# Kernel optimization log

Measured on AMD Instinct MI355X. Metric: run time of the kernel, lower is better.

Reference implementation:

```python
import jax, jax.numpy as jnp
import numpy as np

N = 200_000      # nodes
DEG = 10         # edges per node (RadiusGraph max_num_neighbors=10, loop=True)
E = N * DEG
F0, F1 = 3, 20   # in features (pos), hidden
EPS = 1e-5       # PyG StdAggregation epsilon


def _glorot(k, shape):
    return jax.random.normal(k, shape, jnp.float32) / jnp.sqrt(jnp.float32(shape[-1]))


def setup_inputs() -> dict:
    key = jax.random.key(0)
    ks = jax.random.split(key, 20)
    x = jax.random.normal(ks[0], (N, F0), jnp.float32)
    # each node gets DEG incoming edges: dst structured, src random; first edge per node is a self-loop
    src = jax.random.randint(ks[1], (E,), 0, N, jnp.int32)
    dst = jnp.repeat(jnp.arange(N, dtype=jnp.int32), DEG)
    src = src.at[::DEG].set(jnp.arange(N, dtype=jnp.int32))  # self-loops
    edge_index = jnp.stack([src, dst])
    return {
        "x": x,
        "edge_index": edge_index,
        # conv1: PNAConv(3, 20)
        "w_pre1": _glorot(ks[2], (F0, 2 * F0)), "b_pre1": jnp.zeros((F0,), jnp.float32),
        "w_post1": _glorot(ks[3], (F1, 17 * F0)), "b_post1": jnp.zeros((F1,), jnp.float32),
        "w_lin1": _glorot(ks[4], (F1, F1)), "b_lin1": jnp.zeros((F1,), jnp.float32),
        # conv2: PNAConv(20, 20)
        "w_pre2": _glorot(ks[5], (F1, 2 * F1)), "b_pre2": jnp.zeros((F1,), jnp.float32),
        "w_post2": _glorot(ks[6], (F1, 17 * F1)), "b_post2": jnp.zeros((F1,), jnp.float32),
        "w_lin2": _glorot(ks[7], (F1, F1)), "b_lin2": jnp.zeros((F1,), jnp.float32),
        # final Linear(20, 1)
        "w_out": _glorot(ks[8], (1, F1)), "b_out": jnp.zeros((1,), jnp.float32),
    }


def _pna(x, src, dst, avg_lin, avg_log, w_pre, b_pre, w_post, b_post, w_lin, b_lin):
    n = x.shape[0]
    # message: pre_nn(x_i || x_j)
    h = jnp.concatenate([x[dst], x[src]], axis=-1)          # [E, 2F]
    m = h @ w_pre.T + b_pre                                 # [E, F]
    cnt = jax.ops.segment_sum(jnp.ones(dst.shape[0], jnp.float32), dst, num_segments=n)
    deg = jnp.maximum(cnt, 1.0)                             # [N]
    s = jax.ops.segment_sum(m, dst, num_segments=n)
    s2 = jax.ops.segment_sum(m * m, dst, num_segments=n)
    mean = s / deg[:, None]
    var = jax.nn.relu(s2 / deg[:, None] - mean * mean)
    std = jnp.sqrt(var + EPS)
    has = (cnt > 0.0)[:, None]
    mn = jnp.where(has, jax.ops.segment_min(m, dst, num_segments=n), 0.0)
    mx = jnp.where(has, jax.ops.segment_max(m, dst, num_segments=n), 0.0)
    agg = jnp.concatenate([mean, mn, mx, std], axis=-1)     # [N, 4F]
    # degree scalers: identity, amplification, attenuation, linear
    logd = jnp.log(deg + 1.0)[:, None]
    out = jnp.concatenate([agg,
                           agg * (logd / avg_log),
                           agg * (avg_log / logd),
                           agg * (deg / avg_lin)[:, None]], axis=-1)  # [N, 16F]
    out = jnp.concatenate([x, out], axis=-1)                # [N, 17F]
    out = out @ w_post.T + b_post                           # post_nn
    return out @ w_lin.T + b_lin                            # final tower mixer


def reference(x, edge_index, w_pre1, b_pre1, w_post1, b_post1, w_lin1, b_lin1,
              w_pre2, b_pre2, w_post2, b_post2, w_lin2, b_lin2, w_out, b_out):
    src, dst = edge_index[0], edge_index[1]
    n = x.shape[0]
    cnt = jax.ops.segment_sum(jnp.ones(dst.shape[0], jnp.float32), dst, num_segments=n)
    avg_lin = cnt.mean()                    # avg_deg['lin'] over the degree histogram
    avg_log = jnp.log(cnt + 1.0).mean()     # avg_deg['log']
    h = jax.nn.relu(_pna(x, src, dst, avg_lin, avg_log, w_pre1, b_pre1, w_post1, b_post1, w_lin1, b_lin1))
    h = jax.nn.relu(_pna(h, src, dst, avg_lin, avg_log, w_pre2, b_pre2, w_post2, b_post2, w_lin2, b_lin2))
    return h @ w_out.T + b_out              # [N, 1]
```

## Files before the change

### kernel.cpp

```cpp
#include <hip/hip_runtime.h>
#include <hip/hip_fp16.h>


#define N_NODES 200000
#define NPB 64
#define NBLK (N_NODES / NPB)

#define O_WD1  0
#define O_WA1  64
#define O_B1C  304
#define O_WD2  336
#define O_WA2  736
#define O_B2C  2336
#define O_B2H  4096
#define O_D2H  2004096

__global__ __launch_bounds__(128) void fold_kernel(
    const float* __restrict__ w_pre1, const float* __restrict__ b_pre1,
    const float* __restrict__ w_post1, const float* __restrict__ b_post1,
    const float* __restrict__ w_lin1,  const float* __restrict__ b_lin1,
    const float* __restrict__ w_pre2, const float* __restrict__ b_pre2,
    const float* __restrict__ w_post2, const float* __restrict__ b_post2,
    const float* __restrict__ w_lin2,  const float* __restrict__ b_lin2,
    float* __restrict__ ws)
{
    __shared__ float wl1[20], wl2[20], c1[51], c2s[340];
    __shared__ float swa1[12], swa2[80], s1[3], s2[20];
    const int j = blockIdx.x;
    const int t = threadIdx.x;
    if (t < 20) { wl1[t] = w_lin1[j*20 + t]; wl2[t] = w_lin2[j*20 + t]; }
    __syncthreads();
    for (int c = t; c < 51; c += 128) {
        float a = 0.f;
        #pragma unroll
        for (int k = 0; k < 20; ++k) a += wl1[k] * w_post1[k*51 + c];
        c1[c] = a;
    }
    for (int c = t; c < 340; c += 128) {
        float a = 0.f;
        #pragma unroll
        for (int k = 0; k < 20; ++k) a += wl2[k] * w_post2[k*340 + c];
        c2s[c] = a;
    }
    __syncthreads();
    if (t < 12) swa1[t] = c1[3+t]  + c1[15+t]  + c1[27+t]  + c1[39+t];
    if (t < 80) swa2[t] = c2s[20+t] + c2s[100+t] + c2s[180+t] + c2s[260+t];
    __syncthreads();
    if (t < 3)  s1[t] = swa1[t] + swa1[3+t]  + swa1[6+t];
    if (t < 20) s2[t] = swa2[t] + swa2[20+t] + swa2[40+t];
    if (t < 12) ws[O_WA1 + j*12 + t] = swa1[t];
    if (t < 80) ws[O_WA2 + j*80 + t] = swa2[t];
    __syncthreads();
    if (t < 3) {
        float a = c1[t];
        #pragma unroll
        for (int r = 0; r < 3; ++r) a += s1[r] * w_pre1[r*6 + t];
        ws[O_WD1 + j*3 + t] = a;
    }
    if (t < 20) {
        float a = c2s[t];
        #pragma unroll
        for (int r = 0; r < 20; ++r) a += s2[r] * w_pre2[r*40 + t];
        ws[O_WD2 + j*20 + t] = a;
    }
    if (t == 0) {
        float a = b_lin1[j];
        #pragma unroll
        for (int k = 0; k < 20; ++k) a += wl1[k] * b_post1[k];
        #pragma unroll
        for (int r = 0; r < 3;  ++r) a += s1[r] * b_pre1[r];
        ws[O_B1C + j] = a;
        float b = b_lin2[j];
        #pragma unroll
        for (int k = 0; k < 20; ++k) b += wl2[k] * b_post2[k];
        #pragma unroll
        for (int r = 0; r < 20; ++r) b += s2[r] * b_pre2[r];
        ws[O_B2C + j] = b;
    }
}

__global__ __launch_bounds__(320) void k1_kernel(
    const float* __restrict__ x, const int* __restrict__ src,
    const float* __restrict__ w_pre1, const float* __restrict__ w_pre2,
    const float* __restrict__ ws,
    __half* __restrict__ b2h, __half* __restrict__ d2h)
{
    __shared__ float sM[NPB * 33];
    __shared__ float sAgg[NPB * 13];
    __shared__ float sH1[NPB * 21];
    const int t = threadIdx.x;
    const int node0 = blockIdx.x * NPB;

    const int pil = t & 63;
    const float xi0 = x[(node0+pil)*3+0];
    const float xi1 = x[(node0+pil)*3+1];
    const float xi2 = x[(node0+pil)*3+2];

    #pragma unroll
    for (int p = 0; p < 2; ++p) {
        const int slot = p*320 + t;
        const int il = slot / 10, e = slot - il*10;
        const int sj = __builtin_nontemporal_load(&src[node0*10 + slot]);
        const float xs0 = x[sj*3+0], xs1 = x[sj*3+1], xs2 = x[sj*3+2];
        #pragma unroll
        for (int ff = 0; ff < 3; ++ff) {
            sM[il*33 + e*3 + ff] =
                w_pre1[ff*6+3]*xs0 + w_pre1[ff*6+4]*xs1 + w_pre1[ff*6+5]*xs2;
        }
    }
    __syncthreads();

    if (t < 192) {
        const int il = t / 3, f = t - il*3;
        float sum = 0.f, sq = 0.f, mn = 1e30f, mx = -1e30f;
        #pragma unroll
        for (int e = 0; e < 10; ++e) {
            const float m = sM[il*33 + e*3 + f];
            sum += m; sq += m*m; mn = fminf(mn, m); mx = fmaxf(mx, m);
        }
        const float mean = sum * 0.1f;
        const float var  = fmaxf(sq * 0.1f - mean*mean, 0.f);
        sAgg[il*13 + 0 + f] = mean;
        sAgg[il*13 + 3 + f] = mn;
        sAgg[il*13 + 6 + f] = mx;
        sAgg[il*13 + 9 + f] = sqrtf(var + 1e-5f);
    }
    __syncthreads();

    const int wv = __builtin_amdgcn_readfirstlane(t >> 6);
    const int il = t & 63;
    const int node = node0 + il;
    const int f0 = wv * 4;

    float ag[12];
    #pragma unroll
    for (int k = 0; k < 12; ++k) ag[k] = sAgg[il*13 + k];
    #pragma unroll
    for (int ff = 0; ff < 4; ++ff) {
        const int f = f0 + ff;
        float acc = ws[O_B1C + f]
            + ws[O_WD1 + f*3+0]*xi0 + ws[O_WD1 + f*3+1]*xi1 + ws[O_WD1 + f*3+2]*xi2;
        #pragma unroll
        for (int k = 0; k < 12; ++k) acc += ws[O_WA1 + f*12 + k] * ag[k];
        sH1[il*21 + f] = fmaxf(acc, 0.f);
    }
    __syncthreads();

    float hk[20];
    #pragma unroll
    for (int k = 0; k < 20; ++k) hk[k] = sH1[il*21 + k];
    float vb[4], vd[4];
    #pragma unroll
    for (int ff = 0; ff < 4; ++ff) {
        const int f = f0 + ff;
        float B = 0.f, D = ws[O_B2C + f];
        #pragma unroll
        for (int k = 0; k < 20; ++k) {
            B += w_pre2[f*40 + 20 + k] * hk[k];
            D += ws[O_WD2 + f*20 + k]  * hk[k];
        }
        vb[ff] = B; vd[ff] = D;
    }
    union { __half2 h[2]; unsigned long long u; } pb, pd;
    pb.h[0] = __floats2half2_rn(vb[0], vb[1]);
    pb.h[1] = __floats2half2_rn(vb[2], vb[3]);
    pd.h[0] = __floats2half2_rn(vd[0], vd[1]);
    pd.h[1] = __floats2half2_rn(vd[2], vd[3]);
    __builtin_nontemporal_store(pb.u, (unsigned long long*)&b2h[node*20 + f0]);
    __builtin_nontemporal_store(pd.u, (unsigned long long*)&d2h[node*20 + f0]);
}

__global__ __launch_bounds__(320) void k2_kernel(
    const int* __restrict__ src, const float* __restrict__ ws,
    const __half* __restrict__ b2h, const __half* __restrict__ d2h,
    const float* __restrict__ w_out, const float* __restrict__ b_out,
    float* __restrict__ out)
{
    __shared__ float sAgg[NPB * 81];
    __shared__ int   sSrc[NPB * 10];
    __shared__ float sPart[320];
    const int t = threadIdx.x;
    const int node0 = blockIdx.x * NPB;

    const int pil = t & 63;
    const int pf0 = (t >> 6) * 4;
    union { unsigned long long u; __half2 h[2]; } pdd;
    pdd.u = __builtin_nontemporal_load(
        (const unsigned long long*)&d2h[(node0+pil)*20 + pf0]);

    sSrc[t]       = __builtin_nontemporal_load(&src[node0*10 + t]);
    sSrc[320 + t] = __builtin_nontemporal_load(&src[node0*10 + 320 + t]);
    __syncthreads();

    #pragma unroll
    for (int p = 0; p < 2; ++p) {
        const int idx = p*320 + t;
        const int il = idx / 10, fp = idx - il*10;
        const int f = 2*fp;
        float s0=0.f, s1=0.f, q0=0.f, q1=0.f;
        float mn0=1e30f, mn1=1e30f, mx0=-1e30f, mx1=-1e30f;
        #pragma unroll
        for (int e = 0; e < 10; ++e) {
            const int sj = sSrc[il*10 + e];
            const float2 b = __half22float2(*(const __half2*)&b2h[sj*20 + f]);
            s0 += b.x; q0 += b.x*b.x; mn0 = fminf(mn0, b.x); mx0 = fmaxf(mx0, b.x);
            s1 += b.y; q1 += b.y*b.y; mn1 = fminf(mn1, b.y); mx1 = fmaxf(mx1, b.y);
        }
        const float me0 = s0*0.1f, me1 = s1*0.1f;
        const float sd0 = sqrtf(fmaxf(q0*0.1f - me0*me0, 0.f) + 1e-5f);
        const float sd1 = sqrtf(fmaxf(q1*0.1f - me1*me1, 0.f) + 1e-5f);
        sAgg[il*81 + f]      = me0;  sAgg[il*81 + f + 1]      = me1;
        sAgg[il*81 + 20 + f] = mn0;  sAgg[il*81 + 20 + f + 1] = mn1;
        sAgg[il*81 + 40 + f] = mx0;  sAgg[il*81 + 40 + f + 1] = mx1;
        sAgg[il*81 + 60 + f] = sd0;  sAgg[il*81 + 60 + f + 1] = sd1;
    }
    __syncthreads();

    const int wv = __builtin_amdgcn_readfirstlane(t >> 6);
    const int il = t & 63;
    const int f0 = wv * 4;

    const float2 d01 = __half22float2(pdd.h[0]);
    const float2 d23 = __half22float2(pdd.h[1]);
    float acc0 = d01.x, acc1 = d01.y, acc2 = d23.x, acc3 = d23.y;
    #pragma unroll
    for (int k = 0; k < 80; ++k) {
        const float ag = sAgg[il*81 + k];
        acc0 += ws[O_WA2 + (f0+0)*80 + k] * ag;
        acc1 += ws[O_WA2 + (f0+1)*80 + k] * ag;
        acc2 += ws[O_WA2 + (f0+2)*80 + k] * ag;
        acc3 += ws[O_WA2 + (f0+3)*80 + k] * ag;
    }
    const float py = w_out[f0+0]*fmaxf(acc0, 0.f) + w_out[f0+1]*fmaxf(acc1, 0.f)
                   + w_out[f0+2]*fmaxf(acc2, 0.f) + w_out[f0+3]*fmaxf(acc3, 0.f);
    sPart[wv*64 + il] = py;
    __syncthreads();

    if (t < 64) {
        float y = b_out[0];
        #pragma unroll
        for (int v = 0; v < 5; ++v) y += sPart[v*64 + t];
        __builtin_nontemporal_store(y, &out[node0 + t]);
    }
}

extern "C" void kernel_launch(void* const* d_in, const int* in_sizes, int n_in,
                              void* d_out, int out_size, void* d_ws, size_t ws_size,
                              hipStream_t stream)
{
    const float* x       = (const float*)d_in[0];
    const int*   eidx    = (const int*)  d_in[1];
    const float* w_pre1  = (const float*)d_in[2];
    const float* b_pre1  = (const float*)d_in[3];
    const float* w_post1 = (const float*)d_in[4];
    const float* b_post1 = (const float*)d_in[5];
    const float* w_lin1  = (const float*)d_in[6];
    const float* b_lin1  = (const float*)d_in[7];
    const float* w_pre2  = (const float*)d_in[8];
    const float* b_pre2  = (const float*)d_in[9];
    const float* w_post2 = (const float*)d_in[10];
    const float* b_post2 = (const float*)d_in[11];
    const float* w_lin2  = (const float*)d_in[12];
    const float* b_lin2  = (const float*)d_in[13];
    const float* w_out   = (const float*)d_in[14];
    const float* b_out   = (const float*)d_in[15];
    float* out = (float*)d_out;
    float* ws  = (float*)d_ws;
    __half* b2h = (__half*)(ws + O_B2H);
    __half* d2h = (__half*)(ws + O_D2H);

    fold_kernel<<<20, 128, 0, stream>>>(w_pre1, b_pre1, w_post1, b_post1,
                                        w_lin1, b_lin1, w_pre2, b_pre2,
                                        w_post2, b_post2, w_lin2, b_lin2, ws);
    k1_kernel<<<NBLK, 320, 0, stream>>>(x, eidx, w_pre1, w_pre2, ws, b2h, d2h);
    k2_kernel<<<NBLK, 320, 0, stream>>>(eidx, ws, b2h, d2h, w_out, b_out, out);
}
```

Baseline: 66.40 us.

## Double nodes per block and pad gathered half table rows to 64 bytes

Each block now handles 128 nodes instead of 64, with bounds checks for a partial tail block, so every thread processes two nodes and the weight loads are amortised over more work. The layer-2 gather table b2h is padded from 20 to 32 halves per node, so each neighbour row starts on a 64-byte boundary and the gather in k2 touches fewer cache lines. Nontemporal loads and stores are swapped for plain accesses. In exchange the gather table takes more memory and more store bandwidth, and the larger shared-memory footprint and fewer blocks may lower occupancy.

```diff
diff --git a/kernel.cpp b/kernel.cpp
--- a/kernel.cpp
+++ b/kernel.cpp
@@ -3,8 +3,8 @@
 
 
 #define N_NODES 200000
-#define NPB 64
-#define NBLK (N_NODES / NPB)
+#define NPB 128
+#define NBLK ((N_NODES + NPB - 1) / NPB)
 
 #define O_WD1  0
 #define O_WA1  64
@@ -13,7 +13,7 @@
 #define O_WA2  736
 #define O_B2C  2336
 #define O_B2H  4096
-#define O_D2H  2004096
+#define O_D2H  3204096
 
 __global__ __launch_bounds__(128) void fold_kernel(
     const float* __restrict__ w_pre1, const float* __restrict__ b_pre1,
@@ -90,84 +90,108 @@
     __shared__ float sH1[NPB * 21];
     const int t = threadIdx.x;
     const int node0 = blockIdx.x * NPB;
-
-    const int pil = t & 63;
-    const float xi0 = x[(node0+pil)*3+0];
-    const float xi1 = x[(node0+pil)*3+1];
-    const float xi2 = x[(node0+pil)*3+2];
+    const int nv = (N_NODES - node0 < NPB) ? (N_NODES - node0) : NPB;
+
+    float xi[2][3];
+    #pragma unroll
+    for (int h = 0; h < 2; ++h) {
+        const int n = node0 + h*64 + (t & 63);
+        if (n < N_NODES) {
+            xi[h][0] = x[n*3+0]; xi[h][1] = x[n*3+1]; xi[h][2] = x[n*3+2];
+        }
+    }
+
+    #pragma unroll
+    for (int p = 0; p < 4; ++p) {
+        const int slot = p*320 + t;
+        if (slot < nv*10) {
+            const int il = slot / 10, e = slot - il*10;
+            const int sj = src[node0*10 + slot];
+            const float xs0 = x[sj*3+0], xs1 = x[sj*3+1], xs2 = x[sj*3+2];
+            #pragma unroll
+            for (int ff = 0; ff < 3; ++ff) {
+                sM[il*33 + e*3 + ff] =
+                    w_pre1[ff*6+3]*xs0 + w_pre1[ff*6+4]*xs1 + w_pre1[ff*6+5]*xs2;
+            }
+        }
+    }
+    __syncthreads();
 
     #pragma unroll
     for (int p = 0; p < 2; ++p) {
-        const int slot = p*320 + t;
-        const int il = slot / 10, e = slot - il*10;
-        const int sj = __builtin_nontemporal_load(&src[node0*10 + slot]);
-        const float xs0 = x[sj*3+0], xs1 = x[sj*3+1], xs2 = x[sj*3+2];
-        #pragma unroll
-        for (int ff = 0; ff < 3; ++ff) {
-            sM[il*33 + e*3 + ff] =
-                w_pre1[ff*6+3]*xs0 + w_pre1[ff*6+4]*xs1 + w_pre1[ff*6+5]*xs2;
-        }
-    }
-    __syncthreads();
-
-    if (t < 192) {
-        const int il = t / 3, f = t - il*3;
-        float sum = 0.f, sq = 0.f, mn = 1e30f, mx = -1e30f;
-        #pragma unroll
-        for (int e = 0; e < 10; ++e) {
-            const float m = sM[il*33 + e*3 + f];
-            sum += m; sq += m*m; mn = fminf(mn, m); mx = fmaxf(mx, m);
-        }
-        const float mean = sum * 0.1f;
-        const float var  = fmaxf(sq * 0.1f - mean*mean, 0.f);
-        sAgg[il*13 + 0 + f] = mean;
-        sAgg[il*13 + 3 + f] = mn;
-        sAgg[il*13 + 6 + f] = mx;
-        sAgg[il*13 + 9 + f] = sqrtf(var + 1e-5f);
+        const int idx = p*320 + t;
+        if (idx < nv*3) {
+            const int il = idx / 3, f = idx - il*3;
+            float sum = 0.f, sq = 0.f, mn = 1e30f, mx = -1e30f;
+            #pragma unroll
+            for (int e = 0; e < 10; ++e) {
+                const float m = sM[il*33 + e*3 + f];
+                sum += m; sq += m*m; mn = fminf(mn, m); mx = fmaxf(mx, m);
+            }
+            const float mean = sum * 0.1f;
+            const float var  = fmaxf(sq * 0.1f - mean*mean, 0.f);
+            sAgg[il*13 + 0 + f] = mean;
+            sAgg[il*13 + 3 + f] = mn;
+            sAgg[il*13 + 6 + f] = mx;
+            sAgg[il*13 + 9 + f] = sqrtf(var + 1e-5f);
+        }
     }
     __syncthreads();
 
     const int wv = __builtin_amdgcn_readfirstlane(t >> 6);
-    const int il = t & 63;
-    const int node = node0 + il;
+    const int lane = t & 63;
     const int f0 = wv * 4;
 
-    float ag[12];
-    #pragma unroll
-    for (int k = 0; k < 12; ++k) ag[k] = sAgg[il*13 + k];
-    #pragma unroll
-    for (int ff = 0; ff < 4; ++ff) {
-        const int f = f0 + ff;
-        float acc = ws[O_B1C + f]
-            + ws[O_WD1 + f*3+0]*xi0 + ws[O_WD1 + f*3+1]*xi1 + ws[O_WD1 + f*3+2]*xi2;
-        #pragma unroll
-        for (int k = 0; k < 12; ++k) acc += ws[O_WA1 + f*12 + k] * ag[k];
-        sH1[il*21 + f] = fmaxf(acc, 0.f);
-    }
-    __syncthreads();
-
-    float hk[20];
-    #pragma unroll
-    for (int k = 0; k < 20; ++k) hk[k] = sH1[il*21 + k];
-    float vb[4], vd[4];
-    #pragma unroll
-    for (int ff = 0; ff < 4; ++ff) {
-        const int f = f0 + ff;
-        float B = 0.f, D = ws[O_B2C + f];
-        #pragma unroll
-        for (int k = 0; k < 20; ++k) {
-            B += w_pre2[f*40 + 20 + k] * hk[k];
-            D += ws[O_WD2 + f*20 + k]  * hk[k];
-        }
-        vb[ff] = B; vd[ff] = D;
-    }
-    union { __half2 h[2]; unsigned long long u; } pb, pd;
-    pb.h[0] = __floats2half2_rn(vb[0], vb[1]);
-    pb.h[1] = __floats2half2_rn(vb[2], vb[3]);
-    pd.h[0] = __floats2half2_rn(vd[0], vd[1]);
-    pd.h[1] = __floats2half2_rn(vd[2], vd[3]);
-    __builtin_nontemporal_store(pb.u, (unsigned long long*)&b2h[node*20 + f0]);
-    __builtin_nontemporal_store(pd.u, (unsigned long long*)&d2h[node*20 + f0]);
+    #pragma unroll
+    for (int h = 0; h < 2; ++h) {
+        const int il = h*64 + lane;
+        if (il < nv) {
+            float ag[12];
+            #pragma unroll
+            for (int k = 0; k < 12; ++k) ag[k] = sAgg[il*13 + k];
+            #pragma unroll
+            for (int ff = 0; ff < 4; ++ff) {
+                const int f = f0 + ff;
+                float acc = ws[O_B1C + f]
+                    + ws[O_WD1 + f*3+0]*xi[h][0] + ws[O_WD1 + f*3+1]*xi[h][1]
+                    + ws[O_WD1 + f*3+2]*xi[h][2];
+                #pragma unroll
+                for (int k = 0; k < 12; ++k) acc += ws[O_WA1 + f*12 + k] * ag[k];
+                sH1[il*21 + f] = fmaxf(acc, 0.f);
+            }
+        }
+    }
+    __syncthreads();
+
+    #pragma unroll
+    for (int h = 0; h < 2; ++h) {
+        const int il = h*64 + lane;
+        if (il < nv) {
+            const int node = node0 + il;
+            float hk[20];
+            #pragma unroll
+            for (int k = 0; k < 20; ++k) hk[k] = sH1[il*21 + k];
+            float vb[4], vd[4];
+            #pragma unroll
+            for (int ff = 0; ff < 4; ++ff) {
+                const int f = f0 + ff;
+                float B = 0.f, D = ws[O_B2C + f];
+                #pragma unroll
+                for (int k = 0; k < 20; ++k) {
+                    B += w_pre2[f*40 + 20 + k] * hk[k];
+                    D += ws[O_WD2 + f*20 + k]  * hk[k];
+                }
+                vb[ff] = B; vd[ff] = D;
+            }
+            union { __half2 h2[2]; unsigned long long u; } pb, pd;
+            pb.h2[0] = __floats2half2_rn(vb[0], vb[1]);
+            pb.h2[1] = __floats2half2_rn(vb[2], vb[3]);
+            pd.h2[0] = __floats2half2_rn(vd[0], vd[1]);
+            pd.h2[1] = __floats2half2_rn(vd[2], vd[3]);
+            *(unsigned long long*)&b2h[node*32 + f0] = pb.u;
+            *(unsigned long long*)&d2h[node*20 + f0] = pd.u;
+        }
+    }
 }
 
 __global__ __launch_bounds__(320) void k2_kernel(
@@ -178,69 +202,88 @@
 {
     __shared__ float sAgg[NPB * 81];
     __shared__ int   sSrc[NPB * 10];
-    __shared__ float sPart[320];
+    __shared__ float sPart[5 * NPB];
     const int t = threadIdx.x;
     const int node0 = blockIdx.x * NPB;
-
-    const int pil = t & 63;
-    const int pf0 = (t >> 6) * 4;
-    union { unsigned long long u; __half2 h[2]; } pdd;
-    pdd.u = __builtin_nontemporal_load(
-        (const unsigned long long*)&d2h[(node0+pil)*20 + pf0]);
-
-    sSrc[t]       = __builtin_nontemporal_load(&src[node0*10 + t]);
-    sSrc[320 + t] = __builtin_nontemporal_load(&src[node0*10 + 320 + t]);
-    __syncthreads();
-
-    #pragma unroll
-    for (int p = 0; p < 2; ++p) {
+    const int nv = (N_NODES - node0 < NPB) ? (N_NODES - node0) : NPB;
+    const int lane = t & 63;
+    const int f0p = (t >> 6) * 4;
+
+    union { unsigned long long u; __half2 h2[2]; } pdd[2];
+    #pragma unroll
+    for (int h = 0; h < 2; ++h) {
+        const int n = node0 + h*64 + lane;
+        if (n < N_NODES)
+            pdd[h].u = *(const unsigned long long*)&d2h[n*20 + f0p];
+    }
+
+    #pragma unroll
+    for (int p = 0; p < 4; ++p) {
+        const int slot = p*320 + t;
+        if (slot < nv*10) sSrc[slot] = src[node0*10 + slot];
+    }
+    __syncthreads();
+
+    #pragma unroll
+    for (int p = 0; p < 4; ++p) {
         const int idx = p*320 + t;
-        const int il = idx / 10, fp = idx - il*10;
-        const int f = 2*fp;
-        float s0=0.f, s1=0.f, q0=0.f, q1=0.f;
-        float mn0=1e30f, mn1=1e30f, mx0=-1e30f, mx1=-1e30f;
-        #pragma unroll
-        for (int e = 0; e < 10; ++e) {
-            const int sj = sSrc[il*10 + e];
-            const float2 b = __half22float2(*(const __half2*)&b2h[sj*20 + f]);
-            s0 += b.x; q0 += b.x*b.x; mn0 = fminf(mn0, b.x); mx0 = fmaxf(mx0, b.x);
-            s1 += b.y; q1 += b.y*b.y; mn1 = fminf(mn1, b.y); mx1 = fmaxf(mx1, b.y);
-        }
-        const float me0 = s0*0.1f, me1 = s1*0.1f;
-        const float sd0 = sqrtf(fmaxf(q0*0.1f - me0*me0, 0.f) + 1e-5f);
-        const float sd1 = sqrtf(fmaxf(q1*0.1f - me1*me1, 0.f) + 1e-5f);
-        sAgg[il*81 + f]      = me0;  sAgg[il*81 + f + 1]      = me1;
-        sAgg[il*81 + 20 + f] = mn0;  sAgg[il*81 + 20 + f + 1] = mn1;
-        sAgg[il*81 + 40 + f] = mx0;  sAgg[il*81 + 40 + f + 1] = mx1;
-        sAgg[il*81 + 60 + f] = sd0;  sAgg[il*81 + 60 + f + 1] = sd1;
+        if (idx < nv*10) {
+            const int il = idx / 10, fp = idx - il*10;
+            const int f = 2*fp;
+            float s0=0.f, s1=0.f, q0=0.f, q1=0.f;
+            float mn0=1e30f, mn1=1e30f, mx0=-1e30f, mx1=-1e30f;
+            #pragma unroll
+            for (int e = 0; e < 10; ++e) {
+                const int sj = sSrc[il*10 + e];
+                const float2 b = __half22float2(*(const __half2*)&b2h[sj*32 + f]);
+                s0 += b.x; q0 += b.x*b.x; mn0 = fminf(mn0, b.x); mx0 = fmaxf(mx0, b.x);
+                s1 += b.y; q1 += b.y*b.y; mn1 = fminf(mn1, b.y); mx1 = fmaxf(mx1, b.y);
+            }
+            const float me0 = s0*0.1f, me1 = s1*0.1f;
+            const float sd0 = sqrtf(fmaxf(q0*0.1f - me0*me0, 0.f) + 1e-5f);
+            const float sd1 = sqrtf(fmaxf(q1*0.1f - me1*me1, 0.f) + 1e-5f);
+            sAgg[il*81 + f]      = me0;  sAgg[il*81 + f + 1]      = me1;
+            sAgg[il*81 + 20 + f] = mn0;  sAgg[il*81 + 20 + f + 1] = mn1;
+            sAgg[il*81 + 40 + f] = mx0;  sAgg[il*81 + 40 + f + 1] = mx1;
+            sAgg[il*81 + 60 + f] = sd0;  sAgg[il*81 + 60 + f + 1] = sd1;
+        }
     }
     __syncthreads();
 
     const int wv = __builtin_amdgcn_readfirstlane(t >> 6);
-    const int il = t & 63;
     const int f0 = wv * 4;
 
-    const float2 d01 = __half22float2(pdd.h[0]);
-    const float2 d23 = __half22float2(pdd.h[1]);
-    float acc0 = d01.x, acc1 = d01.y, acc2 = d23.x, acc3 = d23.y;
-    #pragma unroll
-    for (int k = 0; k < 80; ++k) {
-        const float ag = sAgg[il*81 + k];
-        acc0 += ws[O_WA2 + (f0+0)*80 + k] * ag;
-        acc1 += ws[O_WA2 + (f0+1)*80 + k] * ag;
-        acc2 += ws[O_WA2 + (f0+2)*80 + k] * ag;
-        acc3 += ws[O_WA2 + (f0+3)*80 + k] * ag;
-    }
-    const float py = w_out[f0+0]*fmaxf(acc0, 0.f) + w_out[f0+1]*fmaxf(acc1, 0.f)
-                   + w_out[f0+2]*fmaxf(acc2, 0.f) + w_out[f0+3]*fmaxf(acc3, 0.f);
-    sPart[wv*64 + il] = py;
-    __syncthreads();
-
-    if (t < 64) {
-        float y = b_out[0];
-        #pragma unroll
-        for (int v = 0; v < 5; ++v) y += sPart[v*64 + t];
-        __builtin_nontemporal_store(y, &out[node0 + t]);
+    #pragma unroll
+    for (int h = 0; h < 2; ++h) {
+        const int il = h*64 + lane;
+        if (il < nv) {
+            const float2 d01 = __half22float2(pdd[h].h2[0]);
+            const float2 d23 = __half22float2(pdd[h].h2[1]);
+            float acc0 = d01.x, acc1 = d01.y, acc2 = d23.x, acc3 = d23.y;
+            #pragma unroll
+            for (int k = 0; k < 80; ++k) {
+                const float ag = sAgg[il*81 + k];
+                acc0 += ws[O_WA2 + (f0+0)*80 + k] * ag;
+                acc1 += ws[O_WA2 + (f0+1)*80 + k] * ag;
+                acc2 += ws[O_WA2 + (f0+2)*80 + k] * ag;
+                acc3 += ws[O_WA2 + (f0+3)*80 + k] * ag;
+            }
+            const float py = w_out[f0+0]*fmaxf(acc0, 0.f) + w_out[f0+1]*fmaxf(acc1, 0.f)
+                           + w_out[f0+2]*fmaxf(acc2, 0.f) + w_out[f0+3]*fmaxf(acc3, 0.f);
+            sPart[wv*NPB + il] = py;
+        }
+    }
+    __syncthreads();
+
+    #pragma unroll
+    for (int p = 0; p < 1; ++p) {
+        const int il = t;
+        if (il < nv) {
+            float y = b_out[0];
+            #pragma unroll
+            for (int v = 0; v < 5; ++v) y += sPart[v*NPB + il];
+            out[node0 + il] = y;
+        }
     }
 }
 
```

Result: slower. 89.37 us (+34.6%).

## Pad b2h rows to 32 halves and gather 4 features per load in k2

Applied to the files above, without the earlier changes.

The per-node b2h buffer is padded from 20 to 32 halves per row, and the d2h offset is moved to make room. In k2 each thread now handles 4 features of one node with a single 8-byte gather per edge, replacing two passes of 2-feature 4-byte gathers. This cuts gather instruction count and aligns each row to 64 bytes. Nontemporal loads and stores are also replaced with plain accesses, which lets the randomly gathered data stay in cache but enlarges the intermediate buffer.

```diff
diff --git a/kernel.cpp b/kernel.cpp
--- a/kernel.cpp
+++ b/kernel.cpp
@@ -13,7 +13,7 @@
 #define O_WA2  736
 #define O_B2C  2336
 #define O_B2H  4096
-#define O_D2H  2004096
+#define O_D2H  3204096
 
 __global__ __launch_bounds__(128) void fold_kernel(
     const float* __restrict__ w_pre1, const float* __restrict__ b_pre1,
@@ -100,7 +100,7 @@
     for (int p = 0; p < 2; ++p) {
         const int slot = p*320 + t;
         const int il = slot / 10, e = slot - il*10;
-        const int sj = __builtin_nontemporal_load(&src[node0*10 + slot]);
+        const int sj = src[node0*10 + slot];
         const float xs0 = x[sj*3+0], xs1 = x[sj*3+1], xs2 = x[sj*3+2];
         #pragma unroll
         for (int ff = 0; ff < 3; ++ff) {
@@ -161,13 +161,13 @@
         }
         vb[ff] = B; vd[ff] = D;
     }
-    union { __half2 h[2]; unsigned long long u; } pb, pd;
-    pb.h[0] = __floats2half2_rn(vb[0], vb[1]);
-    pb.h[1] = __floats2half2_rn(vb[2], vb[3]);
-    pd.h[0] = __floats2half2_rn(vd[0], vd[1]);
-    pd.h[1] = __floats2half2_rn(vd[2], vd[3]);
-    __builtin_nontemporal_store(pb.u, (unsigned long long*)&b2h[node*20 + f0]);
-    __builtin_nontemporal_store(pd.u, (unsigned long long*)&d2h[node*20 + f0]);
+    union { __half2 h2[2]; unsigned long long u; } pb, pd;
+    pb.h2[0] = __floats2half2_rn(vb[0], vb[1]);
+    pb.h2[1] = __floats2half2_rn(vb[2], vb[3]);
+    pd.h2[0] = __floats2half2_rn(vd[0], vd[1]);
+    pd.h2[1] = __floats2half2_rn(vd[2], vd[3]);
+    *(unsigned long long*)&b2h[node*32 + f0] = pb.u;
+    *(unsigned long long*)&d2h[node*20 + f0] = pd.u;
 }
 
 __global__ __launch_bounds__(320) void k2_kernel(
@@ -184,35 +184,44 @@
 
     const int pil = t & 63;
     const int pf0 = (t >> 6) * 4;
-    union { unsigned long long u; __half2 h[2]; } pdd;
-    pdd.u = __builtin_nontemporal_load(
-        (const unsigned long long*)&d2h[(node0+pil)*20 + pf0]);
-
-    sSrc[t]       = __builtin_nontemporal_load(&src[node0*10 + t]);
-    sSrc[320 + t] = __builtin_nontemporal_load(&src[node0*10 + 320 + t]);
-    __syncthreads();
-
-    #pragma unroll
-    for (int p = 0; p < 2; ++p) {
-        const int idx = p*320 + t;
-        const int il = idx / 10, fp = idx - il*10;
-        const int f = 2*fp;
-        float s0=0.f, s1=0.f, q0=0.f, q1=0.f;
-        float mn0=1e30f, mn1=1e30f, mx0=-1e30f, mx1=-1e30f;
+    union { unsigned long long u; __half2 h2[2]; } pdd;
+    pdd.u = *(const unsigned long long*)&d2h[(node0+pil)*20 + pf0];
+
+    sSrc[t]       = src[node0*10 + t];
+    sSrc[320 + t] = src[node0*10 + 320 + t];
+    __syncthreads();
+
+    {
+        const int il = t / 5, fq = t - (t/5)*5;
+        const int f0 = fq * 4;
+        float s[4]  = {0.f, 0.f, 0.f, 0.f};
+        float q[4]  = {0.f, 0.f, 0.f, 0.f};
+        float mn[4] = {1e30f, 1e30f, 1e30f, 1e30f};
+        float mx[4] = {-1e30f, -1e30f, -1e30f, -1e30f};
         #pragma unroll
         for (int e = 0; e < 10; ++e) {
             const int sj = sSrc[il*10 + e];
-            const float2 b = __half22float2(*(const __half2*)&b2h[sj*20 + f]);
-            s0 += b.x; q0 += b.x*b.x; mn0 = fminf(mn0, b.x); mx0 = fmaxf(mx0, b.x);
-            s1 += b.y; q1 += b.y*b.y; mn1 = fminf(mn1, b.y); mx1 = fmaxf(mx1, b.y);
-        }
-        const float me0 = s0*0.1f, me1 = s1*0.1f;
-        const float sd0 = sqrtf(fmaxf(q0*0.1f - me0*me0, 0.f) + 1e-5f);
-        const float sd1 = sqrtf(fmaxf(q1*0.1f - me1*me1, 0.f) + 1e-5f);
-        sAgg[il*81 + f]      = me0;  sAgg[il*81 + f + 1]      = me1;
-        sAgg[il*81 + 20 + f] = mn0;  sAgg[il*81 + 20 + f + 1] = mn1;
-        sAgg[il*81 + 40 + f] = mx0;  sAgg[il*81 + 40 + f + 1] = mx1;
-        sAgg[il*81 + 60 + f] = sd0;  sAgg[il*81 + 60 + f + 1] = sd1;
+            union { uint2 u; __half2 h2[2]; } v;
+            v.u = *(const uint2*)&b2h[sj*32 + f0];
+            const float2 a = __half22float2(v.h2[0]);
+            const float2 b = __half22float2(v.h2[1]);
+            const float fv[4] = {a.x, a.y, b.x, b.y};
+            #pragma unroll
+            for (int j = 0; j < 4; ++j) {
+                s[j] += fv[j]; q[j] += fv[j]*fv[j];
+                mn[j] = fminf(mn[j], fv[j]); mx[j] = fmaxf(mx[j], fv[j]);
+            }
+        }
+        #pragma unroll
+        for (int j = 0; j < 4; ++j) {
+            const int f = f0 + j;
+            const float me = s[j] * 0.1f;
+            const float sd = sqrtf(fmaxf(q[j]*0.1f - me*me, 0.f) + 1e-5f);
+            sAgg[il*81 + f]      = me;
+            sAgg[il*81 + 20 + f] = mn[j];
+            sAgg[il*81 + 40 + f] = mx[j];
+            sAgg[il*81 + 60 + f] = sd;
+        }
     }
     __syncthreads();
 
@@ -220,8 +229,8 @@
     const int il = t & 63;
     const int f0 = wv * 4;
 
-    const float2 d01 = __half22float2(pdd.h[0]);
-    const float2 d23 = __half22float2(pdd.h[1]);
+    const float2 d01 = __half22float2(pdd.h2[0]);
+    const float2 d23 = __half22float2(pdd.h2[1]);
     float acc0 = d01.x, acc1 = d01.y, acc2 = d23.x, acc3 = d23.y;
     #pragma unroll
     for (int k = 0; k < 80; ++k) {
@@ -240,7 +249,7 @@
         float y = b_out[0];
         #pragma unroll
         for (int v = 0; v < 5; ++v) y += sPart[v*64 + t];
-        __builtin_nontemporal_store(y, &out[node0 + t]);
+        out[node0 + t] = y;
     }
 }
 
```

Measured after the change: 62.72 us. 1.06x faster.
